# Kernel optimization log

Hardware: AMD Instinct MI355X
Metric: run time of the kernel (lower is better)

## Reference

```python
import jax, jax.numpy as jnp
import numpy as np

B, N, K = 32, 2048, 16          # graphs, nodes per graph, knn neighbors
F_IN, F_OUT, P = 32, 64, 3      # feature dims, pos dim


def setup_inputs() -> dict:
    key = jax.random.key(0)
    ks = jax.random.split(key, 6)
    x = jax.random.normal(ks[0], (B * N, F_IN), dtype=jnp.float32)
    pos = jax.random.normal(ks[1], (B * N, P), dtype=jnp.float32)
    # contiguous equal-size graphs: batch[i] = i // N
    batch = (jnp.arange(B * N, dtype=jnp.int32) // N).astype(jnp.int32)
    W_edge = jax.random.normal(ks[2], (2 * F_IN, F_OUT), dtype=jnp.float32) * 0.1
    b_edge = jax.random.normal(ks[3], (F_OUT,), dtype=jnp.float32) * 0.1
    W_nn = jax.random.normal(ks[4], (F_IN, F_OUT), dtype=jnp.float32) * 0.1
    b_nn = jax.random.normal(ks[5], (F_OUT,), dtype=jnp.float32) * 0.1
    return {"x": x, "pos": pos, "W_edge": W_edge, "b_edge": b_edge,
            "W_nn": W_nn, "b_nn": b_nn, "batch": batch}


def reference(x, pos, W_edge, b_edge, W_nn, b_nn, batch):
    # batch is contiguous with N nodes per graph -> reshape to [B, N, .]
    xb = x.reshape(B, N, F_IN)
    pb = pos.reshape(B, N, P)

    # --- knn_graph on pos, per graph (flow='source_to_target') ---
    sq = jnp.sum(pb * pb, axis=-1)                                   # [B, N]
    d2 = sq[:, :, None] + sq[:, None, :] - 2.0 * jnp.einsum('bnd,bmd->bnm', pb, pb)
    d2 = d2 + jnp.eye(N, dtype=d2.dtype) * 1e30                      # exclude self-loops
    _, idx = jax.lax.top_k(-d2, K)                                   # idx[b, i, k] = k-th nearest j of i

    # --- EdgeConv: message = edge_nn(concat(x_i, x_j - x_i)), aggr=max at i ---
    x_j = jnp.take_along_axis(xb, idx.reshape(B, N * K, 1), axis=1).reshape(B, N, K, F_IN)
    x_i = xb[:, :, None, :]                                          # [B, N, 1, F_IN]
    msg = jnp.concatenate([jnp.broadcast_to(x_i, (B, N, K, F_IN)), x_j - x_i], axis=-1)
    h = jax.nn.relu(msg @ W_edge + b_edge)                           # [B, N, K, F_OUT]
    edge_out = jnp.max(h, axis=2)                                    # max-aggregate over neighbors

    # --- skip branch: nn(x) ---
    skip = jax.nn.relu(xb @ W_nn + b_nn)                             # [B, N, F_OUT]

    return (edge_out + skip).reshape(B * N, F_OUT)
```

## Files before the change

kernel.cpp:

```cpp
#include <hip/hip_runtime.h>

#define NB     32
#define NPTS   2048
#define KNN    16
#define FIN    32
#define FOUT   64

typedef __attribute__((ext_vector_type(8))) short bf16x8;
typedef __attribute__((ext_vector_type(4))) float f32x4;

__device__ inline unsigned bf16pk(float lo, float hi) {
    unsigned a = __float_as_uint(lo), b = __float_as_uint(hi);
    a = (a + 0x7fffu + ((a >> 16) & 1u)) >> 16;
    b = (b + 0x7fffu + ((b >> 16) & 1u)) >> 16;
    return (a & 0xffffu) | (b << 16);
}


#define CEA(x, y) { float _t = fminf(x, y); y = fmaxf(x, y); x = _t; }
#define CED(x, y) { float _t = fmaxf(x, y); y = fminf(x, y); x = _t; }

#define BMERGE16(dk) \
    CEA(dk[0],dk[8])  CEA(dk[1],dk[9])  CEA(dk[2],dk[10]) CEA(dk[3],dk[11]) \
    CEA(dk[4],dk[12]) CEA(dk[5],dk[13]) CEA(dk[6],dk[14]) CEA(dk[7],dk[15]) \
    CEA(dk[0],dk[4])  CEA(dk[1],dk[5])  CEA(dk[2],dk[6])  CEA(dk[3],dk[7])  \
    CEA(dk[8],dk[12]) CEA(dk[9],dk[13]) CEA(dk[10],dk[14]) CEA(dk[11],dk[15]) \
    CEA(dk[0],dk[2])  CEA(dk[1],dk[3])  CEA(dk[4],dk[6])  CEA(dk[5],dk[7])  \
    CEA(dk[8],dk[10]) CEA(dk[9],dk[11]) CEA(dk[12],dk[14]) CEA(dk[13],dk[15]) \
    CEA(dk[0],dk[1])  CEA(dk[2],dk[3])  CEA(dk[4],dk[5])  CEA(dk[6],dk[7])  \
    CEA(dk[8],dk[9])  CEA(dk[10],dk[11]) CEA(dk[12],dk[13]) CEA(dk[14],dk[15])

#define NET8(a) \
    CED(a[0],a[1]) CED(a[2],a[3]) CED(a[4],a[5]) CED(a[6],a[7]) \
    CED(a[0],a[2]) CED(a[1],a[3]) CED(a[4],a[6]) CED(a[5],a[7]) \
    CED(a[1],a[2]) CED(a[5],a[6]) \
    CED(a[0],a[4]) CED(a[1],a[5]) CED(a[2],a[6]) CED(a[3],a[7]) \
    CED(a[2],a[4]) CED(a[3],a[5]) \
    CED(a[1],a[2]) CED(a[3],a[4]) CED(a[5],a[6])

__global__ __launch_bounds__(256) void sq_kernel(
    const float* __restrict__ pos, float4* __restrict__ P4)
{
    const int i = blockIdx.x * 256 + threadIdx.x;
    const float px = pos[i*3 + 0];
    const float py = pos[i*3 + 1];
    const float pz = pos[i*3 + 2];
    const float sq = __fadd_rn(__fadd_rn(__fmul_rn(px,px), __fmul_rn(py,py)),
                               __fmul_rn(pz,pz));
    P4[i] = make_float4(px, py, pz, sq);
}

#define CH   8
#define CHL  (NPTS / CH)

#define D2P(C, DST)                                                        \
    {                                                                      \
        float _dot = __fmaf_rn(me.z, (C).z,                                \
                      __fmaf_rn(me.y, (C).y, __fmul_rn(me.x, (C).x)));     \
        DST = __fmaf_rn(-2.0f, _dot, (C).w);                               \
    }

#define SBATCH2(JB, EXCLF)                                                 \
    {                                                                      \
        float a[8], a2[8];                                                 \
        _Pragma("unroll")                                                  \
        for (int i = 0; i < 8; ++i) {                                      \
            const int j = (JB) + i;                                        \
            const float4 c = pb4[j];                                       \
            float d2;                                                      \
            D2P(c, d2)                                                     \
            a[i] = (EXCLF && j == q) ? 1e30f : d2;                         \
        }                                                                  \
        _Pragma("unroll")                                                  \
        for (int i = 0; i < 8; ++i) {                                      \
            const int j = (JB) + 8 + i;                                    \
            const float4 c = pb4[j];                                       \
            float d2;                                                      \
            D2P(c, d2)                                                     \
            a2[i] = (EXCLF && j == q) ? 1e30f : d2;                        \
        }                                                                  \
        NET8(a)                                                            \
        NET8(a2)                                                           \
        _Pragma("unroll")                                                  \
        for (int i = 0; i < 8; ++i) dk[8+i] = fminf(dk[8+i], a[i]);        \
        BMERGE16(dk)                                                       \
        _Pragma("unroll")                                                  \
        for (int i = 0; i < 8; ++i) dk[8+i] = fminf(dk[8+i], a2[i]);       \
        BMERGE16(dk)                                                       \
    }

#define APP(DD, JJ)                                                        \
    if ((DD) <= tthr) {                                                    \
        if ((DD) < tthr) {                                                 \
            if (cntS + cntT >= KNN) --cntT;                                \
            JL[base + cntS * 64 + l] = (JJ);                               \
            ++cntS;                                                        \
        } else if (cntS + cntT < KNN) {                                    \
            JL[base + (KNN - 1 - cntT) * 64 + l] = (JJ);                   \
            ++cntT;                                                        \
        }                                                                  \
    }

#define RESC(JJ, EXCLF)                                                    \
    {                                                                      \
        const float4 c = pb4[(JJ)];                                        \
        float d2;                                                          \
        D2P(c, d2)                                                         \
        if (EXCLF && (JJ) == q) d2 = 1e30f;                                \
        APP(d2, (JJ))                                                      \
    }

__global__ __launch_bounds__(512, 8) void knn_mlp_kernel(
    const float4* __restrict__ P4, const float* __restrict__ x,
    const float* __restrict__ W_edge, const float* __restrict__ b_edge,
    const float* __restrict__ W_nn,   const float* __restrict__ b_nn,
    float* __restrict__ out)
{
    __shared__ float V[CH * KNN * 64];
    __shared__ int   CNTS[CH * 64];
    __shared__ int   IDX[64 * KNN];

    const int b    = blockIdx.x >> 5;
    const int slab = blockIdx.x & 31;
    const int t    = threadIdx.x;
    const int w    = __builtin_amdgcn_readfirstlane(t >> 6);
    const int l    = t & 63;

    {
        const float4* __restrict__ pb4 = P4 + (size_t)b * NPTS;

        const int    q  = slab * 64 + l;
        const float4 me = pb4[q];

        float dk[KNN];
        #pragma unroll
        for (int s = 0; s < KNN; ++s) dk[s] = 1e30f;

        const int j0  = w * CHL;
        const int exw = slab >> 2;
        const int lo  = j0 + (slab & 3) * 64;

        if (w == exw) {
            for (int jb = j0;      jb < lo;        jb += 16) SBATCH2(jb, false)
            for (int jb = lo;      jb < lo + 64;   jb += 16) SBATCH2(jb, true)
            for (int jb = lo + 64; jb < j0 + CHL;  jb += 16) SBATCH2(jb, false)
        } else {
            for (int jb = j0;      jb < j0 + CHL;  jb += 16) SBATCH2(jb, false)
        }

        #pragma unroll
        for (int s = 0; s < KNN; ++s)
            V[(w * KNN + s) * 64 + l] = dk[s];
        __syncthreads();

        for (int c2 = 0; c2 < CH; ++c2) {
            if (c2 == w) continue;
            float v[KNN];
            #pragma unroll
            for (int s2 = 0; s2 < KNN; ++s2)
                v[s2] = V[(c2 * KNN + s2) * 64 + l];
            #pragma unroll
            for (int s = 0; s < KNN; ++s) dk[s] = fminf(dk[s], v[KNN-1-s]);
            BMERGE16(dk)
        }
        const float tthr = dk[KNN-1];
        __syncthreads();

        int* JL = (int*)V;
        const int base = w * KNN * 64;
        int cntS = 0, cntT = 0;
        if (w == exw) {
            for (int j = j0;      j < lo;        ++j) RESC(j, false)
            for (int j = lo;      j < lo + 64;   ++j) RESC(j, true)
            for (int j = lo + 64; j < j0 + CHL;  ++j) RESC(j, false)
        } else {
            for (int j = j0;      j < j0 + CHL;  ++j) RESC(j, false)
        }
        CNTS[w * 64 + l] = cntS | (cntT << 16);
        __syncthreads();

        if (w == 0) {
            int outc = 0;
            for (int c2 = 0; c2 < CH; ++c2) {
                int cs = CNTS[c2 * 64 + l] & 0xffff;
                for (int s2 = 0; s2 < cs && outc < KNN; ++s2)
                    IDX[l * KNN + outc++] = JL[(c2 * KNN + s2) * 64 + l];
            }
            for (int c2 = 0; c2 < CH && outc < KNN; ++c2) {
                int ct = CNTS[c2 * 64 + l] >> 16;
                for (int s2 = 0; s2 < ct && outc < KNN; ++s2)
                    IDX[l * KNN + outc++] =
                        JL[(c2 * KNN + (KNN - 1 - s2)) * 64 + l];
            }
        }
        __syncthreads();
    }

    {
        const int c15 = l & 15;
        const int g   = l >> 4;
        const int ng  = w & 3;
        const int f0  = (w >> 2) * 2;

        float* Zw = V + ng * (16 * 64);

        const int n0    = b * NPTS + slab * 64 + ng * 16;
        const int gbase = b * NPTS;

        int4 Bhi[2], Bd[2], Bn[2];
        #pragma unroll
        for (int ff = 0; ff < 2; ++ff) {
            const int col = 16 * (f0 + ff) + c15;
            unsigned ph[4], pd[4], pn[4];
            #pragma unroll
            for (int d = 0; d < 4; ++d) {
                const int k0 = g * 8 + 2 * d;
                float h0 = W_edge[(FIN + k0)     * FOUT + col];
                float h1 = W_edge[(FIN + k0 + 1) * FOUT + col];
                float l0 = W_edge[k0       * FOUT + col] - h0;
                float l1 = W_edge[(k0 + 1) * FOUT + col] - h1;
                float n0f = W_nn[k0       * FOUT + col];
                float n1f = W_nn[(k0 + 1) * FOUT + col];
                ph[d] = bf16pk(h0, h1);
                pd[d] = bf16pk(l0, l1);
                pn[d] = bf16pk(n0f, n1f);
            }
            Bhi[ff] = make_int4(ph[0], ph[1], ph[2], ph[3]);
            Bd[ff]  = make_int4(pd[0], pd[1], pd[2], pd[3]);
            Bn[ff]  = make_int4(pn[0], pn[1], pn[2], pn[3]);
        }
        float beF[2], bnF[2];
        #pragma unroll
        for (int ff = 0; ff < 2; ++ff) {
            beF[ff] = b_edge[16 * (f0 + ff) + c15];
            bnF[ff] = b_nn[16 * (f0 + ff) + c15];
        }

        const f32x4 zf = {0.f, 0.f, 0.f, 0.f};

        f32x4 baseF[2], skipF[2];
        {
            const float* rp = x + (size_t)(n0 + c15) * FIN + g * 8;
            float4 v0 = *(const float4*)rp;
            float4 v1 = *(const float4*)(rp + 4);
            int4 pk = make_int4(bf16pk(v0.x, v0.y), bf16pk(v0.z, v0.w),
                                bf16pk(v1.x, v1.y), bf16pk(v1.z, v1.w));
            bf16x8 afi = *(bf16x8*)&pk;
            #pragma unroll
            for (int ff = 0; ff < 2; ++ff) {
                baseF[ff] = __builtin_amdgcn_mfma_f32_16x16x32_bf16(
                    afi, *(bf16x8*)&Bd[ff], zf, 0, 0, 0);
                skipF[ff] = __builtin_amdgcn_mfma_f32_16x16x32_bf16(
                    afi, *(bf16x8*)&Bn[ff], zf, 0, 0, 0);
            }
        }

        int nb0 = IDX[(ng * 16 + 0) * KNN + c15];
        const float* rpp = x + (size_t)(gbase + nb0) * FIN + g * 8;
        float4 pv0 = *(const float4*)rpp;
        float4 pv1 = *(const float4*)(rpp + 4);

        #pragma unroll 1
        for (int i = 0; i < 16; ++i) {
            float4 c0 = pv0, c1 = pv1;
            if (i < 15) {
                int nb = IDX[(ng * 16 + i + 1) * KNN + c15];
                const float* rp = x + (size_t)(gbase + nb) * FIN + g * 8;
                pv0 = *(const float4*)rp;
                pv1 = *(const float4*)(rp + 4);
            }
            int4 pk = make_int4(bf16pk(c0.x, c0.y), bf16pk(c0.z, c0.w),
                                bf16pk(c1.x, c1.y), bf16pk(c1.z, c1.w));
            bf16x8 af = *(bf16x8*)&pk;

            float rmax[2];
            #pragma unroll
            for (int ff = 0; ff < 2; ++ff) {
                f32x4 z = __builtin_amdgcn_mfma_f32_16x16x32_bf16(
                    af, *(bf16x8*)&Bhi[ff], zf, 0, 0, 0);
                float m = fmaxf(fmaxf(z[0], z[1]), fmaxf(z[2], z[3]));
                m = fmaxf(m, __shfl_xor(m, 16));
                m = fmaxf(m, __shfl_xor(m, 32));
                rmax[ff] = m;
            }
            if (g < 2)
                Zw[i * 64 + 16 * (f0 + g) + c15] = (g == 0) ? rmax[0] : rmax[1];
        }

        #pragma unroll
        for (int ff = 0; ff < 2; ++ff) {
            #pragma unroll
            for (int reg = 0; reg < 4; ++reg) {
                const int nd = g * 4 + reg;
                float zmax = Zw[nd * 64 + 16 * (f0 + ff) + c15];
                float e  = fmaxf(zmax + baseF[ff][reg] + beF[ff], 0.f);
                float sk = fmaxf(skipF[ff][reg] + bnF[ff], 0.f);
                out[(size_t)(n0 + nd) * FOUT + 16 * (f0 + ff) + c15] = e + sk;
            }
        }
    }
}

extern "C" void kernel_launch(void* const* d_in, const int* in_sizes, int n_in,
                              void* d_out, int out_size, void* d_ws, size_t ws_size,
                              hipStream_t stream) {
    const float* x      = (const float*)d_in[0];
    const float* pos    = (const float*)d_in[1];
    const float* W_edge = (const float*)d_in[2];
    const float* b_edge = (const float*)d_in[3];
    const float* W_nn   = (const float*)d_in[4];
    const float* b_nn   = (const float*)d_in[5];

    float4* P4   = (float4*)d_ws;
    float*  outp = (float*)d_out;

    sq_kernel     <<<NB * NPTS / 256, 256, 0, stream>>>(pos, P4);
    knn_mlp_kernel<<<NB * 32,         512, 0, stream>>>(P4, x, W_edge, b_edge,
                                                        W_nn, b_nn, outp);
}
```

Measured before the change: 205.9 us.

## Restructure edge MLP phase: stage base/skip in LDS, each wave handles all features

The edge MLP phase is split in two. First, base and skip projections for the 64 nodes go into padded LDS buffers. After a barrier, each wave takes 8 nodes across all 64 output features. Each gathered neighbor row is now loaded and converted to bf16 once per node instead of twice across the two feature-half waves, which halves redundant gather traffic and pack work. The cost is an extra __syncthreads, more LDS traffic for E/S, and four MFMAs plus shuffles per iteration. Output stores are now a full contiguous 64-float row per node.

```diff
diff --git a/kernel.cpp b/kernel.cpp
--- a/kernel.cpp
+++ b/kernel.cpp
@@ -110,15 +110,18 @@
         APP(d2, (JJ))                                                      \
     }
 
+#define ESTRIDE 66
+
 __global__ __launch_bounds__(512, 8) void knn_mlp_kernel(
     const float4* __restrict__ P4, const float* __restrict__ x,
     const float* __restrict__ W_edge, const float* __restrict__ b_edge,
     const float* __restrict__ W_nn,   const float* __restrict__ b_nn,
     float* __restrict__ out)
 {
-    __shared__ float V[CH * KNN * 64];
-    __shared__ int   CNTS[CH * 64];
-    __shared__ int   IDX[64 * KNN];
+    __shared__ __attribute__((aligned(16))) char smem[38912];
+    float* V    = (float*)smem;
+    int*   CNTS = (int*)(smem + 32768);
+    int*   IDX  = (int*)(smem + 34816);
 
     const int b    = blockIdx.x >> 5;
     const int slab = blockIdx.x & 31;
@@ -196,86 +199,96 @@
         __syncthreads();
     }
 
+    const int c15 = l & 15;
+    const int g   = l >> 4;
+    const int nbase = b * NPTS + slab * 64;
+    const int gbase = b * NPTS;
+
+    float* E = (float*)smem;
+    float* S = (float*)(smem + 16896);
+
+    const f32x4 zf = {0.f, 0.f, 0.f, 0.f};
+
     {
-        const int c15 = l & 15;
-        const int g   = l >> 4;
-        const int ng  = w & 3;
-        const int f0  = (w >> 2) * 2;
-
-        float* Zw = V + ng * (16 * 64);
-
-        const int n0    = b * NPTS + slab * 64 + ng * 16;
-        const int gbase = b * NPTS;
-
-        int4 Bhi[2], Bd[2], Bn[2];
+        const int ng = w & 3;
+        const int f0 = (w >> 2) * 2;
+
+        const float* rp = x + (size_t)(nbase + ng * 16 + c15) * FIN + g * 8;
+        float4 v0 = *(const float4*)rp;
+        float4 v1 = *(const float4*)(rp + 4);
+        int4 pk = make_int4(bf16pk(v0.x, v0.y), bf16pk(v0.z, v0.w),
+                            bf16pk(v1.x, v1.y), bf16pk(v1.z, v1.w));
+        bf16x8 afi = *(bf16x8*)&pk;
+
         #pragma unroll
         for (int ff = 0; ff < 2; ++ff) {
             const int col = 16 * (f0 + ff) + c15;
-            unsigned ph[4], pd[4], pn[4];
+            unsigned pd[4], pn[4];
             #pragma unroll
             for (int d = 0; d < 4; ++d) {
                 const int k0 = g * 8 + 2 * d;
                 float h0 = W_edge[(FIN + k0)     * FOUT + col];
                 float h1 = W_edge[(FIN + k0 + 1) * FOUT + col];
-                float l0 = W_edge[k0       * FOUT + col] - h0;
-                float l1 = W_edge[(k0 + 1) * FOUT + col] - h1;
-                float n0f = W_nn[k0       * FOUT + col];
-                float n1f = W_nn[(k0 + 1) * FOUT + col];
-                ph[d] = bf16pk(h0, h1);
-                pd[d] = bf16pk(l0, l1);
-                pn[d] = bf16pk(n0f, n1f);
+                pd[d] = bf16pk(W_edge[k0       * FOUT + col] - h0,
+                               W_edge[(k0 + 1) * FOUT + col] - h1);
+                pn[d] = bf16pk(W_nn[k0 * FOUT + col], W_nn[(k0+1) * FOUT + col]);
+            }
+            int4 bd = make_int4(pd[0], pd[1], pd[2], pd[3]);
+            int4 bn = make_int4(pn[0], pn[1], pn[2], pn[3]);
+            f32x4 baseF = __builtin_amdgcn_mfma_f32_16x16x32_bf16(
+                afi, *(bf16x8*)&bd, zf, 0, 0, 0);
+            f32x4 skipF = __builtin_amdgcn_mfma_f32_16x16x32_bf16(
+                afi, *(bf16x8*)&bn, zf, 0, 0, 0);
+            const float be  = b_edge[col];
+            const float bnn = b_nn[col];
+            #pragma unroll
+            for (int reg = 0; reg < 4; ++reg) {
+                const int nd = ng * 16 + g * 4 + reg;
+                E[nd * ESTRIDE + col] = baseF[reg] + be;
+                S[nd * ESTRIDE + col] = fmaxf(skipF[reg] + bnn, 0.f);
+            }
+        }
+    }
+    __syncthreads();
+
+    {
+        const int n0l = w * 8;
+
+        int4 Bhi[4];
+        #pragma unroll
+        for (int ff = 0; ff < 4; ++ff) {
+            const int col = 16 * ff + c15;
+            unsigned ph[4];
+            #pragma unroll
+            for (int d = 0; d < 4; ++d) {
+                const int k0 = g * 8 + 2 * d;
+                ph[d] = bf16pk(W_edge[(FIN + k0)     * FOUT + col],
+                               W_edge[(FIN + k0 + 1) * FOUT + col]);
             }
             Bhi[ff] = make_int4(ph[0], ph[1], ph[2], ph[3]);
-            Bd[ff]  = make_int4(pd[0], pd[1], pd[2], pd[3]);
-            Bn[ff]  = make_int4(pn[0], pn[1], pn[2], pn[3]);
-        }
-        float beF[2], bnF[2];
-        #pragma unroll
-        for (int ff = 0; ff < 2; ++ff) {
-            beF[ff] = b_edge[16 * (f0 + ff) + c15];
-            bnF[ff] = b_nn[16 * (f0 + ff) + c15];
-        }
-
-        const f32x4 zf = {0.f, 0.f, 0.f, 0.f};
-
-        f32x4 baseF[2], skipF[2];
-        {
-            const float* rp = x + (size_t)(n0 + c15) * FIN + g * 8;
-            float4 v0 = *(const float4*)rp;
-            float4 v1 = *(const float4*)(rp + 4);
-            int4 pk = make_int4(bf16pk(v0.x, v0.y), bf16pk(v0.z, v0.w),
-                                bf16pk(v1.x, v1.y), bf16pk(v1.z, v1.w));
-            bf16x8 afi = *(bf16x8*)&pk;
-            #pragma unroll
-            for (int ff = 0; ff < 2; ++ff) {
-                baseF[ff] = __builtin_amdgcn_mfma_f32_16x16x32_bf16(
-                    afi, *(bf16x8*)&Bd[ff], zf, 0, 0, 0);
-                skipF[ff] = __builtin_amdgcn_mfma_f32_16x16x32_bf16(
-                    afi, *(bf16x8*)&Bn[ff], zf, 0, 0, 0);
-            }
-        }
-
-        int nb0 = IDX[(ng * 16 + 0) * KNN + c15];
+        }
+
+        int nb0 = IDX[n0l * KNN + c15];
         const float* rpp = x + (size_t)(gbase + nb0) * FIN + g * 8;
         float4 pv0 = *(const float4*)rpp;
         float4 pv1 = *(const float4*)(rpp + 4);
 
         #pragma unroll 1
-        for (int i = 0; i < 16; ++i) {
+        for (int i = 0; i < 8; ++i) {
             float4 c0 = pv0, c1 = pv1;
-            if (i < 15) {
-                int nb = IDX[(ng * 16 + i + 1) * KNN + c15];
-                const float* rp = x + (size_t)(gbase + nb) * FIN + g * 8;
-                pv0 = *(const float4*)rp;
-                pv1 = *(const float4*)(rp + 4);
-            }
-            int4 pk = make_int4(bf16pk(c0.x, c0.y), bf16pk(c0.z, c0.w),
-                                bf16pk(c1.x, c1.y), bf16pk(c1.z, c1.w));
-            bf16x8 af = *(bf16x8*)&pk;
-
-            float rmax[2];
-            #pragma unroll
-            for (int ff = 0; ff < 2; ++ff) {
+            if (i < 7) {
+                int nb = IDX[(n0l + i + 1) * KNN + c15];
+                const float* rp2 = x + (size_t)(gbase + nb) * FIN + g * 8;
+                pv0 = *(const float4*)rp2;
+                pv1 = *(const float4*)(rp2 + 4);
+            }
+            int4 pk2 = make_int4(bf16pk(c0.x, c0.y), bf16pk(c0.z, c0.w),
+                                 bf16pk(c1.x, c1.y), bf16pk(c1.z, c1.w));
+            bf16x8 af = *(bf16x8*)&pk2;
+
+            float rmax[4];
+            #pragma unroll
+            for (int ff = 0; ff < 4; ++ff) {
                 f32x4 z = __builtin_amdgcn_mfma_f32_16x16x32_bf16(
                     af, *(bf16x8*)&Bhi[ff], zf, 0, 0, 0);
                 float m = fmaxf(fmaxf(z[0], z[1]), fmaxf(z[2], z[3]));
@@ -283,20 +296,12 @@
                 m = fmaxf(m, __shfl_xor(m, 32));
                 rmax[ff] = m;
             }
-            if (g < 2)
-                Zw[i * 64 + 16 * (f0 + g) + c15] = (g == 0) ? rmax[0] : rmax[1];
-        }
-
-        #pragma unroll
-        for (int ff = 0; ff < 2; ++ff) {
-            #pragma unroll
-            for (int reg = 0; reg < 4; ++reg) {
-                const int nd = g * 4 + reg;
-                float zmax = Zw[nd * 64 + 16 * (f0 + ff) + c15];
-                float e  = fmaxf(zmax + baseF[ff][reg] + beF[ff], 0.f);
-                float sk = fmaxf(skipF[ff][reg] + bnF[ff], 0.f);
-                out[(size_t)(n0 + nd) * FOUT + 16 * (f0 + ff) + c15] = e + sk;
-            }
+            float val = (g == 0) ? rmax[0] : (g == 1) ? rmax[1]
+                      : (g == 2) ? rmax[2] : rmax[3];
+            const int nd = n0l + i;
+            float e = fmaxf(val + E[nd * ESTRIDE + g * 16 + c15], 0.f);
+            float s = S[nd * ESTRIDE + g * 16 + c15];
+            out[(size_t)(nbase + nd) * FOUT + g * 16 + c15] = e + s;
         }
     }
 }
```

New measurement: 204.7 us. About the same (-0.6%).
